# Performance work log

Measured on AMD Instinct MI355X. Metric: run time of the kernel, lower is better.

Reference implementation:

```python
import jax, jax.numpy as jnp
import numpy as np

EMBED_DIM = 1024
NUM_HEADS = 16
HEAD_DIM = EMBED_DIM // NUM_HEADS
EPS = 1e-6
B, T = 4, 8192


def setup_inputs() -> dict:
    key = jax.random.key(0)
    ks = jax.random.split(key, 11)
    s = 1.0 / np.sqrt(EMBED_DIM)
    inp = {
        'query': jax.random.normal(ks[0], (B, T, EMBED_DIM), jnp.float32),
        'key': jax.random.normal(ks[1], (B, T, EMBED_DIM), jnp.float32),
        'value': jax.random.normal(ks[2], (B, T, EMBED_DIM), jnp.float32),
        'Wq': jax.random.normal(ks[3], (EMBED_DIM, EMBED_DIM), jnp.float32) * s,
        'bq': jnp.zeros((EMBED_DIM,), jnp.float32),
        'Wk': jax.random.normal(ks[4], (EMBED_DIM, EMBED_DIM), jnp.float32) * s,
        'bk': jnp.zeros((EMBED_DIM,), jnp.float32),
        'Wv': jax.random.normal(ks[5], (EMBED_DIM, EMBED_DIM), jnp.float32) * s,
        'bv': jnp.zeros((EMBED_DIM,), jnp.float32),
        'Wo': jax.random.normal(ks[6], (EMBED_DIM, EMBED_DIM), jnp.float32) * s,
        'bo': jnp.zeros((EMBED_DIM,), jnp.float32),
    }
    return inp


def _feature_map(x):
    return jax.nn.elu(x) + 1.0


def reference(query, key, value, Wq, bq, Wk, bk, Wv, bv, Wo, bo):
    b, t, _ = query.shape
    # projections (torch Linear: x @ W.T + b)
    q = query @ Wq.T + bq
    k = key @ Wk.T + bk
    v = value @ Wv.T + bv
    # split heads -> (b, h, t, d)
    def split(x):
        return x.reshape(b, t, NUM_HEADS, HEAD_DIM).transpose(0, 2, 1, 3)
    q = _feature_map(split(q))
    k = _feature_map(split(k))
    v = split(v)
    k_sum = k.sum(axis=2)                                   # (b,h,d)
    denom = jnp.einsum('bhtd,bhd->bht', q, k_sum) + EPS     # (b,h,t)
    kv = jnp.einsum('bhtd,bhtv->bhdv', k, v)                # (b,h,d,d)
    out = jnp.einsum('bhtd,bhde->bhte', q, kv) / denom[..., None]
    out = out.transpose(0, 2, 1, 3).reshape(b, t, EMBED_DIM)
    return out @ Wo.T + bo
```

## Files before the change

### kernel.cpp

```cpp
#include <hip/hip_runtime.h>
#include <hip/hip_bf16.h>

typedef long long TLONG;
typedef float  f32x4_t  __attribute__((ext_vector_type(4)));
typedef short  s16x8_t  __attribute__((ext_vector_type(8)));
typedef short  s16x4_t  __attribute__((ext_vector_type(4)));
typedef __bf16 bf16x8_t __attribute__((ext_vector_type(8)));

#define MDIM 32768
#define NDIM 1024
#define KDIM 1024
#define EPSV 1e-6f

__device__ __forceinline__ unsigned short f2bf_bits(float f) {
  __hip_bfloat16 h = __float2bfloat16(f);
  return __builtin_bit_cast(unsigned short, h);
}
__device__ __forceinline__ float bf2f(unsigned short u) {
  unsigned int x = ((unsigned int)u) << 16;
  return __builtin_bit_cast(float, x);
}
__device__ __forceinline__ void load_lds16(const void* g, void* l) {
  __builtin_amdgcn_global_load_lds((const __attribute__((address_space(1))) void*)g,
                                   (__attribute__((address_space(3))) void*)l, 16, 0, 0);
}

__global__ __launch_bounds__(256) void convert_f32_bf16(
    const float* __restrict__ in, unsigned short* __restrict__ out, TLONG n) {
  TLONG i = ((TLONG)blockIdx.x * blockDim.x + threadIdx.x) * 8;
  const TLONG stride = (TLONG)gridDim.x * blockDim.x * 8;
  for (; i < n; i += stride) {
    f32x4_t a = *reinterpret_cast<const f32x4_t*>(in + i);
    f32x4_t b = *reinterpret_cast<const f32x4_t*>(in + i + 4);
    s16x8_t o;
    o[0] = (short)f2bf_bits(a[0]); o[1] = (short)f2bf_bits(a[1]);
    o[2] = (short)f2bf_bits(a[2]); o[3] = (short)f2bf_bits(a[3]);
    o[4] = (short)f2bf_bits(b[0]); o[5] = (short)f2bf_bits(b[1]);
    o[6] = (short)f2bf_bits(b[2]); o[7] = (short)f2bf_bits(b[3]);
    *reinterpret_cast<s16x8_t*>(out + i) = o;
  }
}

template <int FMAP, int OUT>
__global__ __launch_bounds__(512, 2) void gemm256(
    const unsigned short* __restrict__ A, const unsigned short* __restrict__ W,
    const float* __restrict__ bias, void* __restrict__ Cout) {
  __shared__ short lds[65536];
  const int bid = blockIdx.x;
  const int swz = (bid & 7) * 64 + (bid >> 3);
  const int mt = swz >> 2;
  const int nt = swz & 3;

  const int tid = threadIdx.x;
  const int lane = tid & 63;
  const int w = tid >> 6;
  const int wr = w >> 2, wc = w & 3;
  const int l15 = lane & 15, lh = lane >> 4;

  const int arow0 = mt * 256, brow0 = nt * 256;

  auto stage = [&](const unsigned short* __restrict__ src, int lbase, int rowbase, int k0) {
#pragma unroll
    for (int i = 0; i < 4; ++i) {
      const int c = i * 512 + tid;
      const int r = c >> 3, ps = c & 7;
      const int sg = ps ^ (r & 7);
      load_lds16(src + (rowbase + r) * KDIM + k0 + sg * 8, &lds[lbase + c * 8]);
    }
  };

  f32x4_t acc[8][4];
#pragma unroll
  for (int m = 0; m < 8; ++m)
#pragma unroll
    for (int n = 0; n < 4; ++n) acc[m][n] = (f32x4_t)0.0f;

  stage(A, 0, arow0, 0);
  stage(W, 16384, brow0, 0);
  stage(A, 32768, arow0, 64);
  stage(W, 49152, brow0, 64);
  asm volatile("s_waitcnt vmcnt(8)" ::: "memory");
  __builtin_amdgcn_sched_barrier(0);
  __builtin_amdgcn_s_barrier();

  s16x8_t a0[4][2], a1[4][2], bf[4][2];

  auto rdA = [&](int pb, int m, int ks) -> s16x8_t {
    const int row = wr * 128 + m * 16 + l15;
    const int off = pb + row * 64 + (((ks * 4 + lh) ^ (row & 7)) * 8);
    return *reinterpret_cast<const s16x8_t*>(&lds[off]);
  };
  auto rdB = [&](int pb, int n, int ks) -> s16x8_t {
    const int row = wc * 64 + n * 16 + l15;
    const int off = pb + 16384 + row * 64 + (((ks * 4 + lh) ^ (row & 7)) * 8);
    return *reinterpret_cast<const s16x8_t*>(&lds[off]);
  };
  auto quad = [&](s16x8_t (&af)[4][2], int mbase, int nlo) {
    __builtin_amdgcn_s_setprio(1);
#pragma unroll
    for (int m = 0; m < 4; ++m)
#pragma unroll
      for (int n = 0; n < 2; ++n)
#pragma unroll
        for (int ks = 0; ks < 2; ++ks)
          acc[mbase + m][nlo + n] = __builtin_amdgcn_mfma_f32_16x16x32_bf16(
              __builtin_bit_cast(bf16x8_t, af[m][ks]),
              __builtin_bit_cast(bf16x8_t, bf[nlo + n][ks]),
              acc[mbase + m][nlo + n], 0, 0, 0);
    __builtin_amdgcn_s_setprio(0);
  };

  for (int kt = 0; kt < 16; ++kt) {
    const int pb = (kt & 1) * 32768;
#pragma unroll
    for (int m = 0; m < 4; ++m)
#pragma unroll
      for (int ks = 0; ks < 2; ++ks) a0[m][ks] = rdA(pb, m, ks);
#pragma unroll
    for (int n = 0; n < 4; ++n)
#pragma unroll
      for (int ks = 0; ks < 2; ++ks) bf[n][ks] = rdB(pb, n, ks);
    quad(a0, 0, 0);
#pragma unroll
    for (int m = 0; m < 4; ++m)
#pragma unroll
      for (int ks = 0; ks < 2; ++ks) a1[m][ks] = rdA(pb, m + 4, ks);
    quad(a0, 0, 2);
    __builtin_amdgcn_sched_barrier(0);
    asm volatile("s_waitcnt lgkmcnt(0)" ::: "memory");
    __builtin_amdgcn_sched_barrier(0);
    __builtin_amdgcn_s_barrier();
    const int k2 = ((kt + 2) & 15) * 64;
    stage(A, pb, arow0, k2);
    quad(a1, 4, 0);
    stage(W, pb + 16384, brow0, k2);
    quad(a1, 4, 2);
    if (kt < 15) {
      __builtin_amdgcn_sched_barrier(0);
      asm volatile("s_waitcnt vmcnt(8)" ::: "memory");
      __builtin_amdgcn_sched_barrier(0);
      __builtin_amdgcn_s_barrier();
    }
  }

#pragma unroll
  for (int n = 0; n < 4; ++n) {
    const int col = nt * 256 + wc * 64 + n * 16 + l15;
    const float bv = bias[col];
#pragma unroll
    for (int m = 0; m < 8; ++m) {
      const int row0 = mt * 256 + wr * 128 + m * 16 + lh * 4;
      if (OUT == 2) {
        const int b = row0 >> 13, tl = row0 & 8191;
        const int h = col >> 6, d = col & 63;
        s16x4_t o;
#pragma unroll
        for (int j = 0; j < 4; ++j) {
          float v = acc[m][n][j] + bv;
          if (FMAP) v = (v > 0.0f) ? (v + 1.0f) : __expf(v);
          o[j] = (short)f2bf_bits(v);
        }
        *reinterpret_cast<s16x4_t*>(
            reinterpret_cast<unsigned short*>(Cout) +
            (((b * 16 + h) * 64 + d) * 8192 + tl)) = o;
      } else {
#pragma unroll
        for (int j = 0; j < 4; ++j) {
          float v = acc[m][n][j] + bv;
          if (FMAP) v = (v > 0.0f) ? (v + 1.0f) : __expf(v);
          if (OUT == 1)
            reinterpret_cast<float*>(Cout)[(row0 + j) * NDIM + col] = v;
          else
            reinterpret_cast<unsigned short*>(Cout)[(row0 + j) * NDIM + col] = f2bf_bits(v);
        }
      }
    }
  }
}

__global__ __launch_bounds__(256) void kv_ksum_mfma(
    const unsigned short* __restrict__ kT, const unsigned short* __restrict__ vT,
    float* __restrict__ kvT, float* __restrict__ ksum) {
  const int bid = blockIdx.x;
  const int bh = bid >> 4, ch = bid & 15;
  const int tid = threadIdx.x;
  const int lane = tid & 63, w = tid >> 6;
  const int l15 = lane & 15, lh = lane >> 4;
  const int dblk = (w >> 1) * 32, eblk = (w & 1) * 32;

  f32x4_t acc[2][2];
#pragma unroll
  for (int m = 0; m < 2; ++m)
#pragma unroll
    for (int n = 0; n < 2; ++n) acc[m][n] = (f32x4_t)0.0f;
  float ks0 = 0.f, ks1 = 0.f;

  const int tbase = ch * 512 + lh * 8;
  const unsigned short* ka = kT + (bh * 64 + dblk + l15) * 8192 + tbase;
  const unsigned short* va = vT + (bh * 64 + eblk + l15) * 8192 + tbase;

  for (int t0 = 0; t0 < 512; t0 += 32) {
    s16x8_t ar[2], br[2];
#pragma unroll
    for (int m = 0; m < 2; ++m)
      ar[m] = *reinterpret_cast<const s16x8_t*>(ka + m * 16 * 8192 + t0);
#pragma unroll
    for (int n = 0; n < 2; ++n)
      br[n] = *reinterpret_cast<const s16x8_t*>(va + n * 16 * 8192 + t0);
#pragma unroll
    for (int m = 0; m < 2; ++m)
#pragma unroll
      for (int n = 0; n < 2; ++n)
        acc[m][n] = __builtin_amdgcn_mfma_f32_16x16x32_bf16(
            __builtin_bit_cast(bf16x8_t, ar[m]),
            __builtin_bit_cast(bf16x8_t, br[n]), acc[m][n], 0, 0, 0);
    if (eblk == 0) {
#pragma unroll
      for (int i = 0; i < 8; ++i) ks0 += bf2f((unsigned short)ar[0][i]);
#pragma unroll
      for (int i = 0; i < 8; ++i) ks1 += bf2f((unsigned short)ar[1][i]);
    }
  }

  if (eblk == 0) {
    ks0 += __shfl_xor(ks0, 16); ks0 += __shfl_xor(ks0, 32);
    ks1 += __shfl_xor(ks1, 16); ks1 += __shfl_xor(ks1, 32);
    if (lh == 0) {
      atomicAdd(&ksum[bh * 64 + dblk + l15], ks0);
      atomicAdd(&ksum[bh * 64 + dblk + 16 + l15], ks1);
    }
  }
#pragma unroll
  for (int n = 0; n < 2; ++n) {
    const int e = eblk + n * 16 + l15;
#pragma unroll
    for (int m = 0; m < 2; ++m) {
      const int d0 = dblk + m * 16 + lh * 4;
#pragma unroll
      for (int j = 0; j < 4; ++j)
        atomicAdd(&kvT[(bh * 64 + e) * 64 + d0 + j], acc[m][n][j]);
    }
  }
}

__global__ __launch_bounds__(256) void attn_apply_kernel(
    const unsigned short* __restrict__ qf, const float* __restrict__ kvT,
    const float* __restrict__ ksum, unsigned short* __restrict__ att) {
  const int bid = blockIdx.x;
  const int swz = (bid & 7) * 256 + (bid >> 3);
  const int bh = swz >> 5;
  const int tile = swz & 31;
  const int b = bh >> 4, h = bh & 15;
  const int tid = threadIdx.x;
  const int lane = tid & 63, w = tid >> 6;
  const int l15 = lane & 15, lh = lane >> 4;

  float ksr[16];
#pragma unroll
  for (int i = 0; i < 16; ++i) ksr[i] = ksum[bh * 64 + lh * 16 + i];

  bf16x8_t bfrag[2][4];
#pragma unroll
  for (int ks2 = 0; ks2 < 2; ++ks2)
#pragma unroll
    for (int n = 0; n < 4; ++n) {
      const float* p = kvT + (bh * 64 + n * 16 + l15) * 64 + ks2 * 32 + lh * 8;
      f32x4_t p0 = *reinterpret_cast<const f32x4_t*>(p);
      f32x4_t p1 = *reinterpret_cast<const f32x4_t*>(p + 4);
      s16x8_t t;
      t[0] = (short)f2bf_bits(p0[0]); t[1] = (short)f2bf_bits(p0[1]);
      t[2] = (short)f2bf_bits(p0[2]); t[3] = (short)f2bf_bits(p0[3]);
      t[4] = (short)f2bf_bits(p1[0]); t[5] = (short)f2bf_bits(p1[1]);
      t[6] = (short)f2bf_bits(p1[2]); t[7] = (short)f2bf_bits(p1[3]);
      bfrag[ks2][n] = __builtin_bit_cast(bf16x8_t, t);
    }

  const int rbase = b * 8192 + tile * 256 + w * 64;
  f32x4_t acc[4][4];
#pragma unroll
  for (int m = 0; m < 4; ++m)
#pragma unroll
    for (int n = 0; n < 4; ++n) acc[m][n] = (f32x4_t)0.0f;
  float rden[4][4];

#pragma unroll
  for (int m = 0; m < 4; ++m) {
    const int row = rbase + m * 16 + l15;
    const unsigned short* qrow = qf + row * 1024 + h * 64;
    bf16x8_t afr[2];
#pragma unroll
    for (int ks2 = 0; ks2 < 2; ++ks2)
      afr[ks2] = __builtin_bit_cast(bf16x8_t,
          *reinterpret_cast<const s16x8_t*>(qrow + ks2 * 32 + lh * 8));
    s16x8_t qa = *reinterpret_cast<const s16x8_t*>(qrow + lh * 16);
    s16x8_t qb = *reinterpret_cast<const s16x8_t*>(qrow + lh * 16 + 8);
    float part = 0.f;
#pragma unroll
    for (int i = 0; i < 8; ++i) part += bf2f((unsigned short)qa[i]) * ksr[i];
#pragma unroll
    for (int i = 0; i < 8; ++i) part += bf2f((unsigned short)qb[i]) * ksr[8 + i];
    part += __shfl_xor(part, 16);
    part += __shfl_xor(part, 32);
#pragma unroll
    for (int j = 0; j < 4; ++j) {
      float dj = __shfl(part, lh * 4 + j);
      rden[m][j] = 1.0f / (dj + EPSV);
    }
#pragma unroll
    for (int ks2 = 0; ks2 < 2; ++ks2)
#pragma unroll
      for (int n = 0; n < 4; ++n)
        acc[m][n] = __builtin_amdgcn_mfma_f32_16x16x32_bf16(afr[ks2], bfrag[ks2][n], acc[m][n], 0, 0, 0);
  }

#pragma unroll
  for (int m = 0; m < 4; ++m)
#pragma unroll
    for (int n = 0; n < 4; ++n) {
      const int col = h * 64 + n * 16 + l15;
#pragma unroll
      for (int j = 0; j < 4; ++j) {
        const int row = rbase + m * 16 + lh * 4 + j;
        att[row * 1024 + col] = f2bf_bits(acc[m][n][j] * rden[m][j]);
      }
    }
}

extern "C" void kernel_launch(void* const* d_in, const int* in_sizes, int n_in,
                              void* d_out, int out_size, void* d_ws, size_t ws_size,
                              hipStream_t stream) {
  const float* query = (const float*)d_in[0];
  const float* key   = (const float*)d_in[1];
  const float* value = (const float*)d_in[2];
  const float* Wq = (const float*)d_in[3];
  const float* bq = (const float*)d_in[4];
  const float* Wk = (const float*)d_in[5];
  const float* bk = (const float*)d_in[6];
  const float* Wv = (const float*)d_in[7];
  const float* bv = (const float*)d_in[8];
  const float* Wo = (const float*)d_in[9];
  const float* bo = (const float*)d_in[10];
  float* out = (float*)d_out;

  if (ws_size < 277889024ULL) return;
  char* ws = (char*)d_ws;
  unsigned short* Vbf = (unsigned short*)(ws + 0);
  unsigned short* qf  = (unsigned short*)(ws + 67108864);
  unsigned short* kTf = (unsigned short*)(ws + 134217728);
  unsigned short* vTf = (unsigned short*)(ws + 201326592);
  unsigned short* Wqb = (unsigned short*)(ws + 268435456);
  unsigned short* Wkb = Wqb + 1048576;
  unsigned short* Wvb = Wkb + 1048576;
  unsigned short* Wob = Wvb + 1048576;
  float* kvT  = (float*)(ws + 276824064);
  float* ksum = (float*)(ws + 277872640);

  unsigned short* Qbf = (unsigned short*)d_out;
  unsigned short* Kbf = Qbf + 33554432;

  hipMemsetAsync(kvT, 0, (size_t)(64 * 64 * 64 + 64 * 64) * sizeof(float), stream);

  convert_f32_bf16<<<2048, 256, 0, stream>>>(query, Qbf, 33554432LL);
  convert_f32_bf16<<<2048, 256, 0, stream>>>(key,   Kbf, 33554432LL);
  convert_f32_bf16<<<2048, 256, 0, stream>>>(value, Vbf, 33554432LL);
  convert_f32_bf16<<<512, 256, 0, stream>>>(Wq, Wqb, 1048576LL);
  convert_f32_bf16<<<512, 256, 0, stream>>>(Wk, Wkb, 1048576LL);
  convert_f32_bf16<<<512, 256, 0, stream>>>(Wv, Wvb, 1048576LL);
  convert_f32_bf16<<<512, 256, 0, stream>>>(Wo, Wob, 1048576LL);

  gemm256<1, 0><<<512, 512, 0, stream>>>(Qbf, Wqb, bq, qf);
  gemm256<1, 2><<<512, 512, 0, stream>>>(Kbf, Wkb, bk, kTf);
  gemm256<0, 2><<<512, 512, 0, stream>>>(Vbf, Wvb, bv, vTf);

  kv_ksum_mfma<<<1024, 256, 0, stream>>>(kTf, vTf, kvT, ksum);

  attn_apply_kernel<<<2048, 256, 0, stream>>>(qf, kvT, ksum, Vbf);

  gemm256<0, 1><<<512, 512, 0, stream>>>(Vbf, Wob, bo, out);
}
```

Measured before the change: 649.4 us.

## Restructure GEMM main loop into 8-phase half-tile staged pipeline

Splits global-to-LDS staging into half-tile chunks and interleaves them with the four MFMA quadrants. A is prefetched two k-steps ahead and W one step ahead, with extra barriers between phases, in the style of hipBLASLt ping-pong schedules. The aim is to spread memory traffic evenly across the compute phases and keep the MFMA units fed. The cost is more barriers, tighter prefetch slack for W, and a risk of LDS hazards if the wait counts are wrong.

```diff
diff --git a/kernel.cpp b/kernel.cpp
--- a/kernel.cpp
+++ b/kernel.cpp
@@ -59,13 +59,14 @@
 
   const int arow0 = mt * 256, brow0 = nt * 256;
 
-  auto stage = [&](const unsigned short* __restrict__ src, int lbase, int rowbase, int k0) {
-#pragma unroll
-    for (int i = 0; i < 4; ++i) {
+  auto stage_half = [&](const unsigned short* __restrict__ src, int ldsOff,
+                        int grow, int k0) {
+#pragma unroll
+    for (int i = 0; i < 2; ++i) {
       const int c = i * 512 + tid;
       const int r = c >> 3, ps = c & 7;
-      const int sg = ps ^ (r & 7);
-      load_lds16(src + (rowbase + r) * KDIM + k0 + sg * 8, &lds[lbase + c * 8]);
+      load_lds16(src + (grow + r) * KDIM + k0 + ((ps ^ (r & 7)) * 8),
+                 &lds[ldsOff + c * 8]);
     }
   };
 
@@ -75,27 +76,19 @@
 #pragma unroll
     for (int n = 0; n < 4; ++n) acc[m][n] = (f32x4_t)0.0f;
 
-  stage(A, 0, arow0, 0);
-  stage(W, 16384, brow0, 0);
-  stage(A, 32768, arow0, 64);
-  stage(W, 49152, brow0, 64);
-  asm volatile("s_waitcnt vmcnt(8)" ::: "memory");
-  __builtin_amdgcn_sched_barrier(0);
-  __builtin_amdgcn_s_barrier();
-
-  s16x8_t a0[4][2], a1[4][2], bf[4][2];
+  s16x8_t Af[8][2], Bf[4][2];
 
   auto rdA = [&](int pb, int m, int ks) -> s16x8_t {
     const int row = wr * 128 + m * 16 + l15;
-    const int off = pb + row * 64 + (((ks * 4 + lh) ^ (row & 7)) * 8);
-    return *reinterpret_cast<const s16x8_t*>(&lds[off]);
+    return *reinterpret_cast<const s16x8_t*>(
+        &lds[pb + row * 64 + (((ks * 4 + lh) ^ (row & 7)) * 8)]);
   };
   auto rdB = [&](int pb, int n, int ks) -> s16x8_t {
     const int row = wc * 64 + n * 16 + l15;
-    const int off = pb + 16384 + row * 64 + (((ks * 4 + lh) ^ (row & 7)) * 8);
-    return *reinterpret_cast<const s16x8_t*>(&lds[off]);
+    return *reinterpret_cast<const s16x8_t*>(
+        &lds[pb + 16384 + row * 64 + (((ks * 4 + lh) ^ (row & 7)) * 8)]);
   };
-  auto quad = [&](s16x8_t (&af)[4][2], int mbase, int nlo) {
+  auto quad = [&](int mb, int nl) {
     __builtin_amdgcn_s_setprio(1);
 #pragma unroll
     for (int m = 0; m < 4; ++m)
@@ -103,44 +96,63 @@
       for (int n = 0; n < 2; ++n)
 #pragma unroll
         for (int ks = 0; ks < 2; ++ks)
-          acc[mbase + m][nlo + n] = __builtin_amdgcn_mfma_f32_16x16x32_bf16(
-              __builtin_bit_cast(bf16x8_t, af[m][ks]),
-              __builtin_bit_cast(bf16x8_t, bf[nlo + n][ks]),
-              acc[mbase + m][nlo + n], 0, 0, 0);
+          acc[mb + m][nl + n] = __builtin_amdgcn_mfma_f32_16x16x32_bf16(
+              __builtin_bit_cast(bf16x8_t, Af[mb + m][ks]),
+              __builtin_bit_cast(bf16x8_t, Bf[nl + n][ks]),
+              acc[mb + m][nl + n], 0, 0, 0);
     __builtin_amdgcn_s_setprio(0);
   };
 
+  stage_half(A, 0,             arow0,       0);
+  stage_half(A, 8192,          arow0 + 128, 0);
+  stage_half(W, 16384,         brow0,       0);
+  stage_half(W, 16384 + 8192,  brow0 + 128, 0);
+  stage_half(A, 32768,         arow0,       64);
+  stage_half(A, 32768 + 8192,  arow0 + 128, 64);
+  asm volatile("s_waitcnt vmcnt(4)" ::: "memory");
+  __builtin_amdgcn_sched_barrier(0);
+  __builtin_amdgcn_s_barrier();
+
+#pragma unroll 2
   for (int kt = 0; kt < 16; ++kt) {
-    const int pb = (kt & 1) * 32768;
+    const int p = kt & 1;
+    const int pb = p * 32768, qb = (1 - p) * 32768;
+    const int k1 = ((kt + 1) & 15) * 64;
+    const int k2 = ((kt + 2) & 15) * 64;
 #pragma unroll
     for (int m = 0; m < 4; ++m)
 #pragma unroll
-      for (int ks = 0; ks < 2; ++ks) a0[m][ks] = rdA(pb, m, ks);
+      for (int ks = 0; ks < 2; ++ks) Af[m][ks] = rdA(pb, m, ks);
 #pragma unroll
     for (int n = 0; n < 4; ++n)
 #pragma unroll
-      for (int ks = 0; ks < 2; ++ks) bf[n][ks] = rdB(pb, n, ks);
-    quad(a0, 0, 0);
-#pragma unroll
-    for (int m = 0; m < 4; ++m)
-#pragma unroll
-      for (int ks = 0; ks < 2; ++ks) a1[m][ks] = rdA(pb, m + 4, ks);
-    quad(a0, 0, 2);
-    __builtin_amdgcn_sched_barrier(0);
+      for (int ks = 0; ks < 2; ++ks) Bf[n][ks] = rdB(pb, n, ks);
+    stage_half(W, qb + 16384, brow0, k1);
+    __builtin_amdgcn_s_barrier();
     asm volatile("s_waitcnt lgkmcnt(0)" ::: "memory");
     __builtin_amdgcn_sched_barrier(0);
-    __builtin_amdgcn_s_barrier();
-    const int k2 = ((kt + 2) & 15) * 64;
-    stage(A, pb, arow0, k2);
-    quad(a1, 4, 0);
-    stage(W, pb + 16384, brow0, k2);
-    quad(a1, 4, 2);
-    if (kt < 15) {
-      __builtin_amdgcn_sched_barrier(0);
-      asm volatile("s_waitcnt vmcnt(8)" ::: "memory");
-      __builtin_amdgcn_sched_barrier(0);
-      __builtin_amdgcn_s_barrier();
-    }
+    quad(0, 0);
+    __builtin_amdgcn_s_barrier();
+#pragma unroll
+    for (int m = 0; m < 4; ++m)
+#pragma unroll
+      for (int ks = 0; ks < 2; ++ks) Af[4 + m][ks] = rdA(pb, 4 + m, ks);
+    stage_half(W, qb + 16384 + 8192, brow0 + 128, k1);
+    __builtin_amdgcn_s_barrier();
+    asm volatile("s_waitcnt lgkmcnt(0)" ::: "memory");
+    __builtin_amdgcn_sched_barrier(0);
+    quad(0, 2);
+    __builtin_amdgcn_s_barrier();
+    stage_half(A, pb, arow0, k2);
+    __builtin_amdgcn_s_barrier();
+    quad(4, 0);
+    __builtin_amdgcn_s_barrier();
+    stage_half(A, pb + 8192, arow0 + 128, k2);
+    __builtin_amdgcn_s_barrier();
+    quad(4, 2);
+    asm volatile("s_waitcnt vmcnt(4)" ::: "memory");
+    __builtin_amdgcn_sched_barrier(0);
+    __builtin_amdgcn_s_barrier();
   }
 
 #pragma unroll
```

Result: slower. 778.4 us (+19.9%).
